# Kernel optimization log

Measured on AMD Instinct MI355X. Metric: run time of the kernel, lower is better.

Reference implementation:

```python
import jax, jax.numpy as jnp
import numpy as np

K, D = 512, 256

def setup_inputs() -> dict:
    key = jax.random.key(0)
    k1, k2 = jax.random.split(key)
    z_e = jax.random.normal(k1, (64, D, 32, 32), dtype=jnp.float32)
    # matches nn.Embedding weight init uniform_(-1/K, 1/K)
    codebook = jax.random.uniform(k2, (K, D), dtype=jnp.float32, minval=-1.0 / K, maxval=1.0 / K)
    return {"z_e": z_e, "codebook": codebook}

def reference(z_e, codebook):
    N, Dd, H, W = z_e.shape
    # NCHW -> (N*H*W, D) tokens
    x = jnp.transpose(z_e, (0, 2, 3, 1)).reshape(-1, Dd)
    x_sq = jnp.sum(x * x, axis=1, keepdims=True)            # [T, 1]
    w_sq = jnp.sum(codebook * codebook, axis=1)             # [K]
    dists = x_sq - 2.0 * (x @ codebook.T) + w_sq[None, :]   # [T, K]
    q = jnp.argmin(dists, axis=1)                           # [T]
    z_q = codebook[q]                                       # [T, D] gather
    z_q = z_q.reshape(N, H, W, Dd).transpose(0, 3, 1, 2)    # back to NCHW
    q = q.reshape(N, H, W).astype(jnp.int64)
    return (q, z_q)
```

## Files before the change

### kernel.cpp

```cpp
#include <hip/hip_runtime.h>
#include <float.h>
#include <math.h>


#define KCODES 512
#define DDIM   256
#define HWSZ   1024
#define TTOK   65536
#define TPB    64
#define NBLK   (TTOK / TPB)
#define NCHUNK 16
#define MARGIN 1.0e-3f

#define HW_OFF 33792
#define BK_OFF 35840
#define LDS_SZ 36096
#define ZQ_PITCH 528

typedef short bf16x8 __attribute__((ext_vector_type(8)));
typedef float f32x16 __attribute__((ext_vector_type(16)));
typedef float f32x4  __attribute__((ext_vector_type(4)));

__device__ inline unsigned short bf16rne(float x) {
    union { float f; unsigned u; } a; a.f = x;
    unsigned r = a.u + (0x7fffu + ((a.u >> 16) & 1u));
    return (unsigned short)(r >> 16);
}
__device__ inline float bf16tof(unsigned short h) {
    union { unsigned u; float f; } b; b.u = ((unsigned)h) << 16; return b.f;
}

__device__ __forceinline__ void top4_insert(float m, int c, float fb[4], int fi[4]) {
    #pragma unroll
    for (int l = 0; l < 4; ++l) {
        const bool s = m > fb[l];
        const float nm = s ? fb[l] : m;
        const int   nc = s ? fi[l] : c;
        fb[l] = s ? m : fb[l];
        fi[l] = s ? c : fi[l];
        m = nm; c = nc;
    }
}
__device__ __forceinline__ void top8_insert(float m, int c, float fb[8], int fi[8]) {
    #pragma unroll
    for (int l = 0; l < 8; ++l) {
        const bool s = m > fb[l];
        const float nm = s ? fb[l] : m;
        const int   nc = s ? fi[l] : c;
        fb[l] = s ? m : fb[l];
        fi[l] = s ? c : fi[l];
        m = nm; c = nc;
    }
}

__global__ __launch_bounds__(256) void vq_prep(const float* __restrict__ cb,
                                               unsigned char* __restrict__ wsw,
                                               float* __restrict__ wsq) {
    const int tid = threadIdx.x;
    const int gid = blockIdx.x * 256 + tid;
    {
        const int k = gid >> 5, o = gid & 31;
        const int d0 = o * 8, c = o >> 1, half = o & 1;
        unsigned hi[4], lo[4];
        #pragma unroll
        for (int jj = 0; jj < 4; ++jj) {
            float v0 = cb[k * DDIM + d0 + 2 * jj];
            float v1 = cb[k * DDIM + d0 + 2 * jj + 1];
            unsigned short h0 = bf16rne(v0), h1 = bf16rne(v1);
            unsigned short l0 = bf16rne(v0 - bf16tof(h0));
            unsigned short l1 = bf16rne(v1 - bf16tof(h1));
            hi[jj] = (unsigned)h0 | ((unsigned)h1 << 16);
            lo[jj] = (unsigned)l0 | ((unsigned)l1 << 16);
        }
        const int tile = k >> 5, lane2 = (k & 31) + 32 * half;
        *(uint4*)(wsw + ((size_t)((c * 2 + 0) * 16 + tile) * 1024) + lane2 * 16) = make_uint4(hi[0], hi[1], hi[2], hi[3]);
        *(uint4*)(wsw + ((size_t)((c * 2 + 1) * 16 + tile) * 1024) + lane2 * 16) = make_uint4(lo[0], lo[1], lo[2], lo[3]);
    }
    if (blockIdx.x < 32) {
        const int k = blockIdx.x * 16 + (tid >> 4);
        const int s = tid & 15, h2 = s >> 3, j2 = s & 7;
        const float* p = cb + (size_t)k * DDIM + h2 * 128 + j2;
        float v[16];
        #pragma unroll
        for (int i = 0; i < 16; ++i) v[i] = p[i * 8];
        float rr;
        {
#pragma clang fp contract(off)
            rr = v[0] * v[0];
            #pragma unroll
            for (int i = 1; i < 16; ++i) { float sq = v[i] * v[i]; rr = rr + sq; }
        }
        float t = rr;
        t = t + __shfl_xor(t, 1);
        t = t + __shfl_xor(t, 2);
        t = t + __shfl_xor(t, 4);
        t = t + __shfl_xor(t, 8);
        if (s == 0) wsq[k] = t;
    }
}

__global__ __launch_bounds__(512, 4) void vq_main(const float* __restrict__ z_e,
                                                  const float* __restrict__ cb,
                                                  const float* __restrict__ wsq,
                                                  const unsigned char* __restrict__ wsw,
                                                  float* __restrict__ out) {
    __shared__ __align__(16) unsigned char lds[LDS_SZ];

    const int tid = threadIdx.x;
    const int wv = tid >> 6, lane = tid & 63;
    const int tbase = blockIdx.x * TPB;
    const int n = tbase >> 10, hw0 = tbase & (HWSZ - 1);
    const float* zb = z_e + (size_t)n * (DDIM * HWSZ) + hw0;

    {
        const int tok = tid & 63, g = tid >> 6;
        const int mtS = tok >> 5;
        const int lbase = (tok & 31) * 16;
        #pragma unroll
        for (int o = 0; o < 4; ++o) {
            const int d0 = g * 32 + o * 8;
            float v[8];
            #pragma unroll
            for (int j = 0; j < 8; ++j) v[j] = zb[(size_t)(d0 + j) * HWSZ + tok];
            unsigned hi[4];
            #pragma unroll
            for (int jj = 0; jj < 4; ++jj) {
                unsigned short h0 = bf16rne(v[2 * jj]), h1 = bf16rne(v[2 * jj + 1]);
                hi[jj] = (unsigned)h0 | ((unsigned)h1 << 16);
            }
            const int c = d0 >> 4;
            const int off2 = lbase + 512 * ((d0 >> 3) & 1);
            *(uint4*)(lds + (mtS * 16 + c) * 1024 + off2) = make_uint4(hi[0], hi[1], hi[2], hi[3]);
        }
    }
    ((float*)(lds + HW_OFF))[tid] = 0.5f * wsq[tid];

    __syncthreads();

    const int hh = lane >> 5;
    const int ct0 = wv * 2;
    const float* hwsqL = (const float*)(lds + HW_OFF);

    #define LDW(c, p, t)   (*(const bf16x8*)(wsw + ((size_t)(((c) * 2 + (p)) * 16 + (t)) * 1024) + lane * 16))
    #define LDA(mm, c)     (*(const bf16x8*)(lds + ((mm) * 16 + (c)) * 1024 + lane * 16))

    float fbA[4] = {-FLT_MAX, -FLT_MAX, -FLT_MAX, -FLT_MAX};
    int   fiA[4] = {KCODES, KCODES, KCODES, KCODES};
    float fbB[4] = {-FLT_MAX, -FLT_MAX, -FLT_MAX, -FLT_MAX};
    int   fiB[4] = {KCODES, KCODES, KCODES, KCODES};

    {
        f32x16 a00, a01, a10, a11;
        #pragma unroll
        for (int r = 0; r < 16; ++r) { a00[r] = 0.f; a01[r] = 0.f; a10[r] = 0.f; a11[r] = 0.f; }
        bf16x8 Xc[2][2], Wc[2][4];
        Xc[0][0] = LDA(0, 0); Xc[0][1] = LDA(1, 0);
        Wc[0][0] = LDW(0, 0, ct0);     Wc[0][1] = LDW(0, 1, ct0);
        Wc[0][2] = LDW(0, 0, ct0 + 1); Wc[0][3] = LDW(0, 1, ct0 + 1);
        #pragma unroll
        for (int c = 0; c < NCHUNK; ++c) {
            const int cur = c & 1, nxt = cur ^ 1;
            if (c + 1 < NCHUNK) {
                Wc[nxt][0] = LDW(c + 1, 0, ct0);     Wc[nxt][1] = LDW(c + 1, 1, ct0);
                Wc[nxt][2] = LDW(c + 1, 0, ct0 + 1); Wc[nxt][3] = LDW(c + 1, 1, ct0 + 1);
                Xc[nxt][0] = LDA(0, c + 1); Xc[nxt][1] = LDA(1, c + 1);
            }
            a00 = __builtin_amdgcn_mfma_f32_32x32x16_bf16(Wc[cur][0], Xc[cur][0], a00, 0, 0, 0);
            a10 = __builtin_amdgcn_mfma_f32_32x32x16_bf16(Wc[cur][0], Xc[cur][1], a10, 0, 0, 0);
            a01 = __builtin_amdgcn_mfma_f32_32x32x16_bf16(Wc[cur][2], Xc[cur][0], a01, 0, 0, 0);
            a11 = __builtin_amdgcn_mfma_f32_32x32x16_bf16(Wc[cur][2], Xc[cur][1], a11, 0, 0, 0);
            a00 = __builtin_amdgcn_mfma_f32_32x32x16_bf16(Wc[cur][1], Xc[cur][0], a00, 0, 0, 0);
            a10 = __builtin_amdgcn_mfma_f32_32x32x16_bf16(Wc[cur][1], Xc[cur][1], a10, 0, 0, 0);
            a01 = __builtin_amdgcn_mfma_f32_32x32x16_bf16(Wc[cur][3], Xc[cur][0], a01, 0, 0, 0);
            a11 = __builtin_amdgcn_mfma_f32_32x32x16_bf16(Wc[cur][3], Xc[cur][1], a11, 0, 0, 0);
        }
        #pragma unroll
        for (int rq = 0; rq < 4; ++rq) {
            const f32x4 h40 = *(const f32x4*)(hwsqL + ct0 * 32 + rq * 8 + 4 * hh);
            const f32x4 h41 = *(const f32x4*)(hwsqL + (ct0 + 1) * 32 + rq * 8 + 4 * hh);
            #pragma unroll
            for (int rr = 0; rr < 4; ++rr) {
                const int code0 = ct0 * 32 + rr + 8 * rq + 4 * hh;
                const int code1 = (ct0 + 1) * 32 + rr + 8 * rq + 4 * hh;
                top4_insert(a00[rq * 4 + rr] - h40[rr], code0, fbA, fiA);
                top4_insert(a01[rq * 4 + rr] - h41[rr], code1, fbA, fiA);
                top4_insert(a10[rq * 4 + rr] - h40[rr], code0, fbB, fiB);
                top4_insert(a11[rq * 4 + rr] - h41[rr], code1, fbB, fiB);
            }
        }
    }

    {
        float sb[4]; int si[4];
        #pragma unroll
        for (int c = 0; c < 4; ++c) { sb[c] = __shfl_xor(fbA[c], 32); si[c] = __shfl_xor(fiA[c], 32); }
        #pragma unroll
        for (int c = 0; c < 4; ++c) top4_insert(sb[c], si[c], fbA, fiA);
        #pragma unroll
        for (int c = 0; c < 4; ++c) { sb[c] = __shfl_xor(fbB[c], 32); si[c] = __shfl_xor(fiB[c], 32); }
        #pragma unroll
        for (int c = 0; c < 4; ++c) top4_insert(sb[c], si[c], fbB, fiB);
    }

    __syncthreads();
    float* candm = (float*)lds;
    int*   candi = (int*)(lds + 8192);
    int*   wlCnt = (int*)(lds + 16384);
    int*   wlTok = (int*)(lds + 16400);
    int*   wlGi  = (int*)(lds + 16656);
    float* wlG   = (float*)(lds + 18704);
    int*   bkArr = (int*)(lds + BK_OFF);
    if (lane < 32) {
        const int slot0 = (wv * 64 + lane) * 4;
        const int slot1 = (wv * 64 + 32 + lane) * 4;
        #pragma unroll
        for (int c = 0; c < 4; ++c) { candm[slot0 + c] = fbA[c]; candi[slot0 + c] = fiA[c]; }
        #pragma unroll
        for (int c = 0; c < 4; ++c) { candm[slot1 + c] = fbB[c]; candi[slot1 + c] = fiB[c]; }
    }
    if (tid == 0) *wlCnt = 0;
    __syncthreads();

    if (tid < TPB) {
        float g[8]; int gi[8];
        #pragma unroll
        for (int c = 0; c < 8; ++c) { g[c] = -FLT_MAX; gi[c] = KCODES; }
        #pragma unroll
        for (int w8 = 0; w8 < 8; ++w8) {
            const int slot = (w8 * 64 + tid) * 4;
            #pragma unroll
            for (int c = 0; c < 4; ++c) top8_insert(candm[slot + c], candi[slot + c], g, gi);
        }
        if (g[0] - g[1] > MARGIN) {
            out[tbase + tid] = (float)gi[0];
            bkArr[tid] = gi[0];
        } else {
            const int slot = atomicAdd(wlCnt, 1);
            wlTok[slot] = tid;
            #pragma unroll
            for (int c = 0; c < 8; ++c) { wlGi[slot * 8 + c] = gi[c]; wlG[slot * 8 + c] = g[c]; }
        }
    }
    __syncthreads();

    {
        const int nIt = *wlCnt;
        for (int it = wv; it < nIt; it += 8) {
            const int tok = wlTok[it];
            const float g0 = wlG[it * 8];
            const float* xa = zb + tok;

            float xsq;
            {
                const int h2 = (lane >> 3) & 1, j2 = lane & 7;
                float v[16];
                if (lane < 16) {
                    #pragma unroll
                    for (int i = 0; i < 16; ++i)
                        v[i] = xa[(size_t)(h2 * 128 + i * 8 + j2) * HWSZ];
                } else {
                    #pragma unroll
                    for (int i = 0; i < 16; ++i) v[i] = 0.f;
                }
                float rr;
                {
#pragma clang fp contract(off)
                    rr = v[0] * v[0];
                    #pragma unroll
                    for (int i = 1; i < 16; ++i) { float sq = v[i] * v[i]; rr = rr + sq; }
                }
                float t = rr;
                t = t + __shfl_xor(t, 1);
                t = t + __shfl_xor(t, 2);
                t = t + __shfl_xor(t, 4);
                t = t + __shfl_xor(t, 8);
                xsq = __shfl(t, 0);
            }

            double xv[4];
            #pragma unroll
            for (int i = 0; i < 4; ++i)
                xv[i] = (double)xa[(size_t)(lane + 64 * i) * HWSZ];

            float bestd = FLT_MAX; int bestk = KCODES;
            for (int c = 0; c < 8; ++c) {
                const float gc = wlG[it * 8 + c];
                if (c > 0 && g0 - gc > MARGIN) break;
                const int idx = wlGi[it * 8 + c];
                const float* wr = cb + (size_t)idx * DDIM;
                double A = 0.0;
                #pragma unroll
                for (int i = 0; i < 4; ++i)
                    A = fma((double)wr[lane + 64 * i], xv[i], A);
                A = A + __shfl_xor(A, 1);
                A = A + __shfl_xor(A, 2);
                A = A + __shfl_xor(A, 4);
                A = A + __shfl_xor(A, 8);
                A = A + __shfl_xor(A, 16);
                A = A + __shfl_xor(A, 32);
                float dist;
                {
#pragma clang fp contract(off)
                    const float xw = (float)A;
                    const float t1 = xsq - 2.0f * xw;
                    dist = t1 + wsq[idx];
                }
                if (dist < bestd || (dist == bestd && idx < bestk)) { bestd = dist; bestk = idx; }
            }
            if (lane == 0) {
                out[tbase + tok] = (float)bestk;
                bkArr[tok] = bestk;
            }
        }
    }

    #pragma unroll
    for (int r = 0; r < 2; ++r) {
        __syncthreads();
        {
            #pragma unroll
            for (int rr = 0; rr < 8; ++rr) {
                const int row = wv * 8 + rr;
                const int bk = bkArr[row];
                const float2 vv = *(const float2*)(cb + (size_t)bk * DDIM + r * 128 + lane * 2);
                *(float2*)(lds + row * ZQ_PITCH + lane * 8) = vv;
            }
        }
        __syncthreads();
        {
            const int tk = tid & 63, s = tid >> 6;
            float* zq = out + TTOK + (size_t)n * (DDIM * HWSZ) + hw0 + tk;
            #pragma unroll
            for (int i = 0; i < 16; i += 4) {
                const f32x4 v = *(const f32x4*)(lds + tk * ZQ_PITCH + (s * 16 + i) * 4);
                #pragma unroll
                for (int j = 0; j < 4; ++j)
                    zq[(size_t)(r * 128 + s * 16 + i + j) * HWSZ] = v[j];
            }
        }
    }
}

extern "C" void kernel_launch(void* const* d_in, const int* in_sizes, int n_in,
                              void* d_out, int out_size, void* d_ws, size_t ws_size,
                              hipStream_t stream) {
    const float* z_e = (const float*)d_in[0];
    const float* cb  = (const float*)d_in[1];
    float* out = (float*)d_out;
    float* wsq = (float*)d_ws;
    unsigned char* wsw = (unsigned char*)d_ws + 2048;

    vq_prep<<<64, 256, 0, stream>>>(cb, wsw, wsq);
    vq_main<<<NBLK, 512, 0, stream>>>(z_e, cb, wsq, wsw, out);
}
```

Before: 185.8 us.

## Process 128 tokens per block and pack top-k candidates into sortable keys

Doubles tokens per block to 128, so each wave runs two MFMA passes over the codebook tiles. Codebook weight loads are amortized over more tokens and the block count is halved. Top-k tracking now uses single 32-bit keys that pack an order-preserving float with the 9-bit code index, replacing separate float/int select chains. The exact-recheck margin is also tightened, which sends fewer tokens to the fp64 fallback at some risk to correctness. LDS usage roughly doubles (~68KB), which may reduce occupancy.

```diff
diff --git a/kernel.cpp b/kernel.cpp
--- a/kernel.cpp
+++ b/kernel.cpp
@@ -7,14 +7,18 @@
 #define DDIM   256
 #define HWSZ   1024
 #define TTOK   65536
-#define TPB    64
+#define TPB    128
 #define NBLK   (TTOK / TPB)
 #define NCHUNK 16
-#define MARGIN 1.0e-3f
-
-#define HW_OFF 33792
-#define BK_OFF 35840
-#define LDS_SZ 36096
+#define MARGIN 3.0e-4f
+#define KINIT  0x00800000u
+
+#define HW_OFF 65536
+#define BK_OFF 67584
+#define LDS_SZ 68096
+#define WLC_OFF 49152
+#define WLT_OFF 49168
+#define WLK_OFF 49680
 #define ZQ_PITCH 528
 
 typedef short bf16x8 __attribute__((ext_vector_type(8)));
@@ -30,26 +34,31 @@
     union { unsigned u; float f; } b; b.u = ((unsigned)h) << 16; return b.f;
 }
 
-__device__ __forceinline__ void top4_insert(float m, int c, float fb[4], int fi[4]) {
+__device__ inline unsigned enc_key(float f, int code) {
+    unsigned s = __float_as_uint(f);
+    unsigned u = (s & 0x80000000u) ? ~s : (s | 0x80000000u);
+    return (u & 0xFFFFFE00u) | (unsigned)code;
+}
+__device__ inline float dec_key(unsigned k) {
+    unsigned u = k & 0xFFFFFE00u;
+    unsigned s = (u & 0x80000000u) ? (u & 0x7FFFFFFFu) : ~u;
+    return __uint_as_float(s);
+}
+
+__device__ __forceinline__ void top4k(unsigned k, unsigned kb[4]) {
     #pragma unroll
     for (int l = 0; l < 4; ++l) {
-        const bool s = m > fb[l];
-        const float nm = s ? fb[l] : m;
-        const int   nc = s ? fi[l] : c;
-        fb[l] = s ? m : fb[l];
-        fi[l] = s ? c : fi[l];
-        m = nm; c = nc;
-    }
-}
-__device__ __forceinline__ void top8_insert(float m, int c, float fb[8], int fi[8]) {
+        const unsigned mx = k > kb[l] ? k : kb[l];
+        const unsigned mn = k > kb[l] ? kb[l] : k;
+        kb[l] = mx; k = mn;
+    }
+}
+__device__ __forceinline__ void top8k(unsigned k, unsigned kb[8]) {
     #pragma unroll
     for (int l = 0; l < 8; ++l) {
-        const bool s = m > fb[l];
-        const float nm = s ? fb[l] : m;
-        const int   nc = s ? fi[l] : c;
-        fb[l] = s ? m : fb[l];
-        fi[l] = s ? c : fi[l];
-        m = nm; c = nc;
+        const unsigned mx = k > kb[l] ? k : kb[l];
+        const unsigned mn = k > kb[l] ? kb[l] : k;
+        kb[l] = mx; k = mn;
     }
 }
 
@@ -113,12 +122,12 @@
     const float* zb = z_e + (size_t)n * (DDIM * HWSZ) + hw0;
 
     {
-        const int tok = tid & 63, g = tid >> 6;
+        const int tok = tid & 127, g = tid >> 7;
         const int mtS = tok >> 5;
         const int lbase = (tok & 31) * 16;
         #pragma unroll
-        for (int o = 0; o < 4; ++o) {
-            const int d0 = g * 32 + o * 8;
+        for (int o = 0; o < 8; ++o) {
+            const int d0 = g * 64 + o * 8;
             float v[8];
             #pragma unroll
             for (int j = 0; j < 8; ++j) v[j] = zb[(size_t)(d0 + j) * HWSZ + tok];
@@ -140,105 +149,102 @@
     const int hh = lane >> 5;
     const int ct0 = wv * 2;
     const float* hwsqL = (const float*)(lds + HW_OFF);
+    unsigned* candp = (unsigned*)lds;
 
     #define LDW(c, p, t)   (*(const bf16x8*)(wsw + ((size_t)(((c) * 2 + (p)) * 16 + (t)) * 1024) + lane * 16))
     #define LDA(mm, c)     (*(const bf16x8*)(lds + ((mm) * 16 + (c)) * 1024 + lane * 16))
 
-    float fbA[4] = {-FLT_MAX, -FLT_MAX, -FLT_MAX, -FLT_MAX};
-    int   fiA[4] = {KCODES, KCODES, KCODES, KCODES};
-    float fbB[4] = {-FLT_MAX, -FLT_MAX, -FLT_MAX, -FLT_MAX};
-    int   fiB[4] = {KCODES, KCODES, KCODES, KCODES};
-
-    {
-        f32x16 a00, a01, a10, a11;
-        #pragma unroll
-        for (int r = 0; r < 16; ++r) { a00[r] = 0.f; a01[r] = 0.f; a10[r] = 0.f; a11[r] = 0.f; }
-        bf16x8 Xc[2][2], Wc[2][4];
-        Xc[0][0] = LDA(0, 0); Xc[0][1] = LDA(1, 0);
-        Wc[0][0] = LDW(0, 0, ct0);     Wc[0][1] = LDW(0, 1, ct0);
-        Wc[0][2] = LDW(0, 0, ct0 + 1); Wc[0][3] = LDW(0, 1, ct0 + 1);
-        #pragma unroll
-        for (int c = 0; c < NCHUNK; ++c) {
-            const int cur = c & 1, nxt = cur ^ 1;
-            if (c + 1 < NCHUNK) {
-                Wc[nxt][0] = LDW(c + 1, 0, ct0);     Wc[nxt][1] = LDW(c + 1, 1, ct0);
-                Wc[nxt][2] = LDW(c + 1, 0, ct0 + 1); Wc[nxt][3] = LDW(c + 1, 1, ct0 + 1);
-                Xc[nxt][0] = LDA(0, c + 1); Xc[nxt][1] = LDA(1, c + 1);
-            }
-            a00 = __builtin_amdgcn_mfma_f32_32x32x16_bf16(Wc[cur][0], Xc[cur][0], a00, 0, 0, 0);
-            a10 = __builtin_amdgcn_mfma_f32_32x32x16_bf16(Wc[cur][0], Xc[cur][1], a10, 0, 0, 0);
-            a01 = __builtin_amdgcn_mfma_f32_32x32x16_bf16(Wc[cur][2], Xc[cur][0], a01, 0, 0, 0);
-            a11 = __builtin_amdgcn_mfma_f32_32x32x16_bf16(Wc[cur][2], Xc[cur][1], a11, 0, 0, 0);
-            a00 = __builtin_amdgcn_mfma_f32_32x32x16_bf16(Wc[cur][1], Xc[cur][0], a00, 0, 0, 0);
-            a10 = __builtin_amdgcn_mfma_f32_32x32x16_bf16(Wc[cur][1], Xc[cur][1], a10, 0, 0, 0);
-            a01 = __builtin_amdgcn_mfma_f32_32x32x16_bf16(Wc[cur][3], Xc[cur][0], a01, 0, 0, 0);
-            a11 = __builtin_amdgcn_mfma_f32_32x32x16_bf16(Wc[cur][3], Xc[cur][1], a11, 0, 0, 0);
-        }
-        #pragma unroll
-        for (int rq = 0; rq < 4; ++rq) {
-            const f32x4 h40 = *(const f32x4*)(hwsqL + ct0 * 32 + rq * 8 + 4 * hh);
-            const f32x4 h41 = *(const f32x4*)(hwsqL + (ct0 + 1) * 32 + rq * 8 + 4 * hh);
-            #pragma unroll
-            for (int rr = 0; rr < 4; ++rr) {
-                const int code0 = ct0 * 32 + rr + 8 * rq + 4 * hh;
-                const int code1 = (ct0 + 1) * 32 + rr + 8 * rq + 4 * hh;
-                top4_insert(a00[rq * 4 + rr] - h40[rr], code0, fbA, fiA);
-                top4_insert(a01[rq * 4 + rr] - h41[rr], code1, fbA, fiA);
-                top4_insert(a10[rq * 4 + rr] - h40[rr], code0, fbB, fiB);
-                top4_insert(a11[rq * 4 + rr] - h41[rr], code1, fbB, fiB);
-            }
-        }
-    }
-
-    {
-        float sb[4]; int si[4];
-        #pragma unroll
-        for (int c = 0; c < 4; ++c) { sb[c] = __shfl_xor(fbA[c], 32); si[c] = __shfl_xor(fiA[c], 32); }
-        #pragma unroll
-        for (int c = 0; c < 4; ++c) top4_insert(sb[c], si[c], fbA, fiA);
-        #pragma unroll
-        for (int c = 0; c < 4; ++c) { sb[c] = __shfl_xor(fbB[c], 32); si[c] = __shfl_xor(fiB[c], 32); }
-        #pragma unroll
-        for (int c = 0; c < 4; ++c) top4_insert(sb[c], si[c], fbB, fiB);
-    }
-
+    unsigned kA[4], kB[4];
+    #pragma unroll
+    for (int pass = 0; pass < 2; ++pass) {
+        const int mtA = 2 * pass, mtB = 2 * pass + 1;
+        #pragma unroll
+        for (int c = 0; c < 4; ++c) { kA[c] = KINIT; kB[c] = KINIT; }
+        {
+            f32x16 a00, a01, a10, a11;
+            #pragma unroll
+            for (int r = 0; r < 16; ++r) { a00[r] = 0.f; a01[r] = 0.f; a10[r] = 0.f; a11[r] = 0.f; }
+            bf16x8 Xc[2][2], Wc[2][4];
+            Xc[0][0] = LDA(mtA, 0); Xc[0][1] = LDA(mtB, 0);
+            Wc[0][0] = LDW(0, 0, ct0);     Wc[0][1] = LDW(0, 1, ct0);
+            Wc[0][2] = LDW(0, 0, ct0 + 1); Wc[0][3] = LDW(0, 1, ct0 + 1);
+            #pragma unroll
+            for (int c = 0; c < NCHUNK; ++c) {
+                const int cur = c & 1, nxt = cur ^ 1;
+                if (c + 1 < NCHUNK) {
+                    Wc[nxt][0] = LDW(c + 1, 0, ct0);     Wc[nxt][1] = LDW(c + 1, 1, ct0);
+                    Wc[nxt][2] = LDW(c + 1, 0, ct0 + 1); Wc[nxt][3] = LDW(c + 1, 1, ct0 + 1);
+                    Xc[nxt][0] = LDA(mtA, c + 1); Xc[nxt][1] = LDA(mtB, c + 1);
+                }
+                a00 = __builtin_amdgcn_mfma_f32_32x32x16_bf16(Wc[cur][0], Xc[cur][0], a00, 0, 0, 0);
+                a10 = __builtin_amdgcn_mfma_f32_32x32x16_bf16(Wc[cur][0], Xc[cur][1], a10, 0, 0, 0);
+                a01 = __builtin_amdgcn_mfma_f32_32x32x16_bf16(Wc[cur][2], Xc[cur][0], a01, 0, 0, 0);
+                a11 = __builtin_amdgcn_mfma_f32_32x32x16_bf16(Wc[cur][2], Xc[cur][1], a11, 0, 0, 0);
+                a00 = __builtin_amdgcn_mfma_f32_32x32x16_bf16(Wc[cur][1], Xc[cur][0], a00, 0, 0, 0);
+                a10 = __builtin_amdgcn_mfma_f32_32x32x16_bf16(Wc[cur][1], Xc[cur][1], a10, 0, 0, 0);
+                a01 = __builtin_amdgcn_mfma_f32_32x32x16_bf16(Wc[cur][3], Xc[cur][0], a01, 0, 0, 0);
+                a11 = __builtin_amdgcn_mfma_f32_32x32x16_bf16(Wc[cur][3], Xc[cur][1], a11, 0, 0, 0);
+            }
+            #pragma unroll
+            for (int rq = 0; rq < 4; ++rq) {
+                const f32x4 h40 = *(const f32x4*)(hwsqL + ct0 * 32 + rq * 8 + 4 * hh);
+                const f32x4 h41 = *(const f32x4*)(hwsqL + (ct0 + 1) * 32 + rq * 8 + 4 * hh);
+                #pragma unroll
+                for (int rr = 0; rr < 4; ++rr) {
+                    const int code0 = ct0 * 32 + rr + 8 * rq + 4 * hh;
+                    const int code1 = (ct0 + 1) * 32 + rr + 8 * rq + 4 * hh;
+                    top4k(enc_key(a00[rq * 4 + rr] - h40[rr], code0), kA);
+                    top4k(enc_key(a01[rq * 4 + rr] - h41[rr], code1), kA);
+                    top4k(enc_key(a10[rq * 4 + rr] - h40[rr], code0), kB);
+                    top4k(enc_key(a11[rq * 4 + rr] - h41[rr], code1), kB);
+                }
+            }
+        }
+        {
+            unsigned sb[4];
+            #pragma unroll
+            for (int c = 0; c < 4; ++c) sb[c] = __shfl_xor((int)kA[c], 32);
+            #pragma unroll
+            for (int c = 0; c < 4; ++c) top4k(sb[c], kA);
+            #pragma unroll
+            for (int c = 0; c < 4; ++c) sb[c] = __shfl_xor((int)kB[c], 32);
+            #pragma unroll
+            for (int c = 0; c < 4; ++c) top4k(sb[c], kB);
+        }
+        if (pass == 0) __syncthreads();
+        if (lane < 32) {
+            const int tokA = mtA * 32 + lane, tokB = mtB * 32 + lane;
+            *(uint4*)(candp + (wv * 128 + tokA) * 4) = make_uint4(kA[0], kA[1], kA[2], kA[3]);
+            *(uint4*)(candp + (wv * 128 + tokB) * 4) = make_uint4(kB[0], kB[1], kB[2], kB[3]);
+        }
+    }
     __syncthreads();
-    float* candm = (float*)lds;
-    int*   candi = (int*)(lds + 8192);
-    int*   wlCnt = (int*)(lds + 16384);
-    int*   wlTok = (int*)(lds + 16400);
-    int*   wlGi  = (int*)(lds + 16656);
-    float* wlG   = (float*)(lds + 18704);
-    int*   bkArr = (int*)(lds + BK_OFF);
-    if (lane < 32) {
-        const int slot0 = (wv * 64 + lane) * 4;
-        const int slot1 = (wv * 64 + 32 + lane) * 4;
-        #pragma unroll
-        for (int c = 0; c < 4; ++c) { candm[slot0 + c] = fbA[c]; candi[slot0 + c] = fiA[c]; }
-        #pragma unroll
-        for (int c = 0; c < 4; ++c) { candm[slot1 + c] = fbB[c]; candi[slot1 + c] = fiB[c]; }
-    }
+
+    int*      wlCnt = (int*)(lds + WLC_OFF);
+    int*      wlTok = (int*)(lds + WLT_OFF);
+    unsigned* wlK   = (unsigned*)(lds + WLK_OFF);
+    int*      bkArr = (int*)(lds + BK_OFF);
     if (tid == 0) *wlCnt = 0;
     __syncthreads();
 
     if (tid < TPB) {
-        float g[8]; int gi[8];
-        #pragma unroll
-        for (int c = 0; c < 8; ++c) { g[c] = -FLT_MAX; gi[c] = KCODES; }
+        unsigned kk[8];
+        #pragma unroll
+        for (int c = 0; c < 8; ++c) kk[c] = KINIT;
         #pragma unroll
         for (int w8 = 0; w8 < 8; ++w8) {
-            const int slot = (w8 * 64 + tid) * 4;
-            #pragma unroll
-            for (int c = 0; c < 4; ++c) top8_insert(candm[slot + c], candi[slot + c], g, gi);
-        }
-        if (g[0] - g[1] > MARGIN) {
-            out[tbase + tid] = (float)gi[0];
-            bkArr[tid] = gi[0];
+            const uint4 q4 = *(const uint4*)(candp + (w8 * 128 + tid) * 4);
+            top8k(q4.x, kk); top8k(q4.y, kk); top8k(q4.z, kk); top8k(q4.w, kk);
+        }
+        const float g0 = dec_key(kk[0]), g1 = dec_key(kk[1]);
+        if (g0 - g1 > MARGIN) {
+            out[tbase + tid] = (float)(kk[0] & 511u);
+            bkArr[tid] = (int)(kk[0] & 511u);
         } else {
             const int slot = atomicAdd(wlCnt, 1);
             wlTok[slot] = tid;
             #pragma unroll
-            for (int c = 0; c < 8; ++c) { wlGi[slot * 8 + c] = gi[c]; wlG[slot * 8 + c] = g[c]; }
+            for (int c = 0; c < 8; ++c) wlK[slot * 8 + c] = kk[c];
         }
     }
     __syncthreads();
@@ -247,7 +253,7 @@
         const int nIt = *wlCnt;
         for (int it = wv; it < nIt; it += 8) {
             const int tok = wlTok[it];
-            const float g0 = wlG[it * 8];
+            const float g0 = dec_key(wlK[it * 8]);
             const float* xa = zb + tok;
 
             float xsq;
@@ -284,9 +290,10 @@
 
             float bestd = FLT_MAX; int bestk = KCODES;
             for (int c = 0; c < 8; ++c) {
-                const float gc = wlG[it * 8 + c];
+                const unsigned kc = wlK[it * 8 + c];
+                const float gc = dec_key(kc);
                 if (c > 0 && g0 - gc > MARGIN) break;
-                const int idx = wlGi[it * 8 + c];
+                const int idx = (int)(kc & 511u);
                 const float* wr = cb + (size_t)idx * DDIM;
                 double A = 0.0;
                 #pragma unroll
@@ -315,27 +322,29 @@
     }
 
     #pragma unroll
-    for (int r = 0; r < 2; ++r) {
+    for (int r = 0; r < 4; ++r) {
+        const int rg = (r & 1) * 64;
+        const int dh = (r >> 1) * 128;
         __syncthreads();
         {
             #pragma unroll
             for (int rr = 0; rr < 8; ++rr) {
                 const int row = wv * 8 + rr;
-                const int bk = bkArr[row];
-                const float2 vv = *(const float2*)(cb + (size_t)bk * DDIM + r * 128 + lane * 2);
+                const int bk = bkArr[rg + row];
+                const float2 vv = *(const float2*)(cb + (size_t)bk * DDIM + dh + lane * 2);
                 *(float2*)(lds + row * ZQ_PITCH + lane * 8) = vv;
             }
         }
         __syncthreads();
         {
             const int tk = tid & 63, s = tid >> 6;
-            float* zq = out + TTOK + (size_t)n * (DDIM * HWSZ) + hw0 + tk;
+            float* zq = out + TTOK + (size_t)n * (DDIM * HWSZ) + hw0 + rg + tk;
             #pragma unroll
             for (int i = 0; i < 16; i += 4) {
                 const f32x4 v = *(const f32x4*)(lds + tk * ZQ_PITCH + (s * 16 + i) * 4);
                 #pragma unroll
                 for (int j = 0; j < 4; ++j)
-                    zq[(size_t)(r * 128 + s * 16 + i + j) * HWSZ] = v[j];
+                    zq[(size_t)(dh + s * 16 + i + j) * HWSZ] = v[j];
             }
         }
     }
```

New measurement: 205.6 us. 1.11x slower.
